# Performance work log

Hardware: AMD Instinct MI355X
Metric: run time of the kernel (lower is better)

## Reference

```python
import jax, jax.numpy as jnp
import numpy as np

KERNEL_MUL = 2.0
KERNEL_NUM = 5


def setup_inputs() -> dict:
    key = jax.random.key(0)
    k1, k2 = jax.random.split(key)
    source = jax.random.normal(k1, (4096, 1024), dtype=jnp.float32)
    target = jax.random.normal(k2, (4096, 1024), dtype=jnp.float32)
    return {"source": source, "target": target}


def reference(source, target):
    bs = source.shape[0]
    total = jnp.concatenate([source, target], axis=0)  # [n, D]
    n = total.shape[0]
    # Pairwise squared L2 distances via the GEMM trick: ||a-b||^2 = a^2 + b^2 - 2ab
    sq = jnp.sum(total * total, axis=1)                 # [n]
    L2 = sq[:, None] + sq[None, :] - 2.0 * (total @ total.T)  # [n, n]
    # Bandwidth computed from detached distances (torch used .data => stop_gradient)
    bw = jax.lax.stop_gradient(L2).sum() / (n * n - n)
    bw = bw / (KERNEL_MUL ** (KERNEL_NUM // 2))
    bws = bw * (KERNEL_MUL ** jnp.arange(KERNEL_NUM, dtype=L2.dtype))  # [K]
    # Multi-bandwidth Gaussian kernel sum: [K, n, n] -> [n, n]
    K = jnp.exp(-L2[None, :, :] / bws[:, None, None]).sum(axis=0)
    XX = K[:bs, :bs].mean()
    YY = K[bs:, bs:].mean()
    XY = K[:bs, bs:].mean()
    YX = K[bs:, :bs].mean()
    return XX + YY - XY - YX
```

## Files before the change

kernel.cpp:

```cpp
#include <hip/hip_runtime.h>
#include <hip/hip_bf16.h>
#include <stdint.h>
#include <stddef.h>

#define NTOT 8192
#define BS   4096
#define DIM  1024
#define NTRI 2080
#define QS   20.0f

#define OFF_TB      0u
#define OFF_SQ      8388608u
#define OFF_COLPART 8421376u
#define OFF_COLP2   10518528u
#define OFF_BWP     10551296u
#define OFF_PART    10551360u


typedef __attribute__((ext_vector_type(4)))  int   i32x4;
typedef __attribute__((ext_vector_type(16))) int   i32x16;

__device__ __forceinline__ float fast_sqrt(float x) {
#if __has_builtin(__builtin_amdgcn_sqrtf)
  return __builtin_amdgcn_sqrtf(x);
#else
  float r; asm("v_sqrt_f32 %0, %1" : "=v"(r) : "v"(x)); return r;
#endif
}

__device__ __forceinline__ float fast_exp2(float x) {
#if __has_builtin(__builtin_amdgcn_exp2f)
  return __builtin_amdgcn_exp2f(x);
#else
  float r; asm("v_exp_f32 %0, %1" : "=v"(r) : "v"(x)); return r;
#endif
}

__device__ __forceinline__ void load_lds16(const void* g, void* l) {
  __builtin_amdgcn_global_load_lds((const __attribute__((address_space(1))) void*)g,
                                   (__attribute__((address_space(3))) void*)l,
                                   16, 0, 0);
}

__device__ __forceinline__ int quant4(float4 v) {
  int q0 = __float2int_rn(fminf(fmaxf(v.x * QS, -127.f), 127.f));
  int q1 = __float2int_rn(fminf(fmaxf(v.y * QS, -127.f), 127.f));
  int q2 = __float2int_rn(fminf(fmaxf(v.z * QS, -127.f), 127.f));
  int q3 = __float2int_rn(fminf(fmaxf(v.w * QS, -127.f), 127.f));
  return (q0 & 255) | ((q1 & 255) << 8) | ((q2 & 255) << 16) | ((q3 & 255) << 24);
}

__global__ __launch_bounds__(256) void prep_kernel(const float* __restrict__ src,
                                                   const float* __restrict__ tgt,
                                                   unsigned char* __restrict__ tb,
                                                   float* __restrict__ sq,
                                                   float* __restrict__ colpart) {
  const int t = threadIdx.x;
  const int lane = t & 63, wave = t >> 6;
  const int R = blockIdx.x;
  const int r0 = R * 16;
  const int kt = t >> 4, kq = (t >> 2) & 3, b0 = (t & 3) * 4;
  unsigned char* dstbase = tb + (size_t)R * 16384 + kt * 1024 + kq * 256 + b0;
  __shared__ float rs[16][4];
  float c0 = 0.f, c1 = 0.f, c2 = 0.f, c3 = 0.f;
#pragma unroll 4
  for (int r = 0; r < 16; ++r) {
    const int row = r0 + r;
    const float* base = (row < BS) ? (src + (size_t)row * DIM)
                                   : (tgt + (size_t)(row - BS) * DIM);
    float4 v = *reinterpret_cast<const float4*>(base + t * 4);
    *reinterpret_cast<int*>(dstbase + r * 16) = quant4(v);
    c0 += v.x; c1 += v.y; c2 += v.z; c3 += v.w;
    float s = v.x*v.x + v.y*v.y + v.z*v.z + v.w*v.w;
#pragma unroll
    for (int off = 32; off > 0; off >>= 1) s += __shfl_down(s, off, 64);
    if (lane == 0) rs[r][wave] = s;
  }
  float4 cp = {c0, c1, c2, c3};
  *reinterpret_cast<float4*>(colpart + (size_t)R * 1024 + t * 4) = cp;
  __syncthreads();
  if (t < 16) sq[r0 + t] = (rs[t][0] + rs[t][1]) + (rs[t][2] + rs[t][3]);
}

__global__ __launch_bounds__(1024) void colred_kernel(const float* __restrict__ colpart,
                                                      float* __restrict__ colp2) {
  const int b = blockIdx.x, t = threadIdx.x;
  float s = 0.f;
  for (int g = b * 64; g < b * 64 + 64; ++g) s += colpart[(size_t)g * 1024 + t];
  colp2[b * 1024 + t] = s;
}

__global__ __launch_bounds__(1024) void bw_kernel(const float* __restrict__ sq,
                                                  const float* __restrict__ colp2,
                                                  float* __restrict__ bwp) {
  const int t = threadIdx.x;
  double s1 = 0.0;
#pragma unroll
  for (int i = 0; i < 8; ++i) s1 += (double)sq[t + i * 1024];
  float s = 0.f;
#pragma unroll
  for (int j = 0; j < 8; ++j) s += colp2[j * 1024 + t];
  double s2 = (double)s * (double)s;
  __shared__ double r1[1024], r2[1024];
  r1[t] = s1; r2[t] = s2;
  __syncthreads();
  for (int off = 512; off > 0; off >>= 1) {
    if (t < off) { r1[t] += r1[t + off]; r2[t] += r2[t + off]; }
    __syncthreads();
  }
  if (t == 0) {
    const double n = (double)NTOT;
    double sumL2 = 2.0 * n * r1[0] - 2.0 * r2[0];
    double bw = sumL2 / (n * n - n);
    bw = bw / 4.0;
    const double LOG2E = 1.4426950408889634;
    for (int k = 0; k < 5; ++k)
      bwp[k] = (float)(-LOG2E / (bw * (double)(1 << k)));
  }
}

#define STAGE(kt1024, ldsA, ldsB)                                             \
  do {                                                                        \
    load_lds16(T + a0g + (kt1024), (ldsA) + (size_t)(wave * 64) * 16);        \
    load_lds16(T + a1g + (kt1024), (ldsA) + (size_t)(256 + wave * 64) * 16);  \
    load_lds16(T + b0g + (kt1024), (ldsB) + (size_t)(wave * 64) * 16);        \
    load_lds16(T + b1g + (kt1024), (ldsB) + (size_t)(256 + wave * 64) * 16);  \
  } while (0)

#define COMPUTE64(Abuf, Bbuf)                                                 \
  do {                                                                        \
    _Pragma("unroll")                                                         \
    for (int kk = 0; kk < 2; ++kk) {                                          \
      i32x4 fa0 = *reinterpret_cast<const i32x4*>(&(Abuf)[abase + kk * 512]); \
      i32x4 fa1 = *reinterpret_cast<const i32x4*>(&(Abuf)[abase + 2048 + kk * 512]); \
      i32x4 fb0 = *reinterpret_cast<const i32x4*>(&(Bbuf)[bbase + kk * 512]); \
      i32x4 fb1 = *reinterpret_cast<const i32x4*>(&(Bbuf)[bbase + 2048 + kk * 512]); \
      acc00 = __builtin_amdgcn_mfma_i32_32x32x32_i8(fa0, fb0, acc00, 0, 0, 0); \
      acc01 = __builtin_amdgcn_mfma_i32_32x32x32_i8(fa0, fb1, acc01, 0, 0, 0); \
      acc10 = __builtin_amdgcn_mfma_i32_32x32x32_i8(fa1, fb0, acc10, 0, 0, 0); \
      acc11 = __builtin_amdgcn_mfma_i32_32x32x32_i8(fa1, fb1, acc11, 0, 0, 0); \
    }                                                                         \
  } while (0)

#define BARR __builtin_amdgcn_s_barrier()

#define EXP5(x16) ({ float u_ = fast_exp2(x16);                               \
                     float u2_ = u_ * u_, u4_ = u2_ * u2_;                    \
                     float u8_ = u4_ * u4_, u16_ = u8_ * u8_;                 \
                     ((u_ + u2_) + (u4_ + u8_)) + u16_; })

__global__ __launch_bounds__(256, 4) void mmd_gemm(const unsigned char* __restrict__ T,
                                                   const float* __restrict__ sq,
                                                   const float* __restrict__ bwp,
                                                   float* __restrict__ partials) {
  __shared__ __align__(16) unsigned char sA0[8192], sA1[8192];
  __shared__ __align__(16) unsigned char sB0[8192], sB1[8192];
  __shared__ float wred[4];

  const int tid  = threadIdx.x;
  const int lane = tid & 63;
  const int wave = tid >> 6;
  const int wr   = wave >> 1;
  const int wc   = wave & 1;
  const int bid  = blockIdx.x;

  const int col5 = lane & 31;
  const int hi32 = lane >> 5;
  const int abase0 = (col5 >> 4) * 1024 + hi32 * 256 + (lane & 15) * 16;
  const int abase = wr * 4096 + abase0;
  const int bbase = wc * 4096 + abase0;

  const int nrep = (bid < 32) ? 2 : 1;
  for (int rep = 0; rep < nrep; ++rep) {
    int tno;
    if (bid < 32) tno = bid * 2 + rep;
    else { const int idx = bid - 32; tno = 64 + (idx & 7) * 252 + (idx >> 3); }

    int bi = (int)((129.0f - fast_sqrt(129.0f * 129.0f - 8.0f * (float)tno)) * 0.5f);
    while (bi > 0 && bi * (129 - bi) / 2 > tno) --bi;
    while ((bi + 1) * (129 - (bi + 1)) / 2 <= tno) ++bi;
    const int bj = bi + (tno - bi * (129 - bi) / 2);

    const int aRB = bi * 8, bRB = bj * 8;
    const int f0 = tid, f1 = 256 + tid;
    const size_t a0g = (size_t)(aRB + (f0 >> 6)) * 16384 + (f0 & 63) * 16;
    const size_t a1g = (size_t)(aRB + (f1 >> 6)) * 16384 + (f1 & 63) * 16;
    const size_t b0g = (size_t)(bRB + (f0 >> 6)) * 16384 + (f0 & 63) * 16;
    const size_t b1g = (size_t)(bRB + (f1 >> 6)) * 16384 + (f1 & 63) * 16;

    i32x16 acc00 = {}, acc01 = {}, acc10 = {}, acc11 = {};

    STAGE(0, sA0, sB0);

    for (int t = 0; t < 8; ++t) {
      STAGE((2 * t + 1) * 1024, sA1, sB1);
      asm volatile("s_waitcnt vmcnt(4)" ::: "memory");
      BARR;
      __builtin_amdgcn_sched_barrier(0);
      COMPUTE64(sA0, sB0);
      __builtin_amdgcn_sched_barrier(0);
      BARR;

      if (t < 7) {
        STAGE((2 * t + 2) * 1024, sA0, sB0);
        asm volatile("s_waitcnt vmcnt(4)" ::: "memory");
      } else {
        asm volatile("s_waitcnt vmcnt(0)" ::: "memory");
      }
      BARR;
      __builtin_amdgcn_sched_barrier(0);
      COMPUTE64(sA1, sB1);
      __builtin_amdgcn_sched_barrier(0);
      BARR;
    }

    const float s16 = bwp[0] * 0.0625f;
    const float c2i = -2.f * s16 / (QS * QS);

    const float bj0 = sq[bj * 128 + wc * 64 + col5] * s16;
    const float bj1 = sq[bj * 128 + wc * 64 + 32 + col5] * s16;

    float tsum = 0.f;
#pragma unroll
    for (int tm = 0; tm < 2; ++tm) {
      const int rbaseq = bi * 128 + wr * 64 + tm * 32 + 4 * hi32;
#pragma unroll
      for (int q = 0; q < 4; ++q) {
#pragma unroll
        for (int p = 0; p < 4; ++p) {
          const float ai = sq[rbaseq + q * 8 + p] * s16;
          const int r = q * 4 + p;
          const int v0 = tm ? acc10[r] : acc00[r];
          const int v1 = tm ? acc11[r] : acc01[r];
          tsum += EXP5(fmaf((float)v0, c2i, ai + bj0));
          tsum += EXP5(fmaf((float)v1, c2i, ai + bj1));
        }
      }
    }

#pragma unroll
    for (int off = 32; off > 0; off >>= 1) tsum += __shfl_down(tsum, off, 64);
    if (lane == 0) wred[wave] = tsum;
    __syncthreads();
    if (tid == 0) {
      float sign = ((bi < 32) == (bj < 32)) ? 1.f : -1.f;
      float wgt  = (bi == bj) ? 1.f : 2.f;
      partials[tno] = sign * wgt * ((wred[0] + wred[1]) + (wred[2] + wred[3]));
    }
    __syncthreads();
  }
}

__global__ __launch_bounds__(256) void finish_kernel(const float* __restrict__ partials,
                                                     float* __restrict__ out) {
  const int t = threadIdx.x;
  double s = 0.0;
  for (int i = t; i < NTRI; i += 256) s += (double)partials[i];
  __shared__ double rd[256];
  rd[t] = s;
  __syncthreads();
  for (int off = 128; off > 0; off >>= 1) {
    if (t < off) rd[t] += rd[t + off];
    __syncthreads();
  }
  if (t == 0) out[0] = (float)(rd[0] / 16777216.0);
}

extern "C" void kernel_launch(void* const* d_in, const int* in_sizes, int n_in,
                              void* d_out, int out_size, void* d_ws, size_t ws_size,
                              hipStream_t stream) {
  const float* src = (const float*)d_in[0];
  const float* tgt = (const float*)d_in[1];
  char* ws = (char*)d_ws;
  unsigned char* tb = (unsigned char*)(ws + OFF_TB);
  float* sq       = (float*)(ws + OFF_SQ);
  float* colpart  = (float*)(ws + OFF_COLPART);
  float* colp2    = (float*)(ws + OFF_COLP2);
  float* bwp      = (float*)(ws + OFF_BWP);
  float* partials = (float*)(ws + OFF_PART);

  prep_kernel<<<dim3(512), dim3(256), 0, stream>>>(src, tgt, tb, sq, colpart);
  colred_kernel<<<dim3(8), dim3(1024), 0, stream>>>(colpart, colp2);
  bw_kernel<<<dim3(1), dim3(1024), 0, stream>>>(sq, colp2, bwp);
  mmd_gemm<<<dim3(2048), dim3(256), 0, stream>>>(tb, sq, bwp, partials);
  finish_kernel<<<dim3(1), dim3(256), 0, stream>>>(partials, (float*)d_out);
}
```

Measured before the change: 76.83 us.

## Enlarge GEMM tile to 256x128 over block-row pairs of the triangle

The tile shape moves from 128x128 to 256x128, and tiles are enumerated over pairs of block rows of the symmetric upper triangle. Each wave now holds a 4x2 grid of MFMA accumulators, which raises arithmetic intensity per LDS byte and halves the number of workgroups. Sub-tiles below the diagonal are computed but skipped in the exp epilogue, and the per-wave sign and weight replace the per-block ones. In exchange, register and LDS use grow, occupancy drops to 2 blocks per CU, and some MFMA work below the diagonal is wasted.

```diff
diff --git a/kernel.cpp b/kernel.cpp
--- a/kernel.cpp
+++ b/kernel.cpp
@@ -6,7 +6,7 @@
 #define NTOT 8192
 #define BS   4096
 #define DIM  1024
-#define NTRI 2080
+#define NT2  1056
 #define QS   20.0f
 
 #define OFF_TB      0u
@@ -121,24 +121,33 @@
 
 #define STAGE(kt1024, ldsA, ldsB)                                             \
   do {                                                                        \
-    load_lds16(T + a0g + (kt1024), (ldsA) + (size_t)(wave * 64) * 16);        \
-    load_lds16(T + a1g + (kt1024), (ldsA) + (size_t)(256 + wave * 64) * 16);  \
-    load_lds16(T + b0g + (kt1024), (ldsB) + (size_t)(wave * 64) * 16);        \
-    load_lds16(T + b1g + (kt1024), (ldsB) + (size_t)(256 + wave * 64) * 16);  \
+    load_lds16(T + ga0 + (kt1024), (ldsA) + (size_t)(wave * 64) * 16);        \
+    load_lds16(T + ga1 + (kt1024), (ldsA) + (size_t)(256 + wave * 64) * 16);  \
+    load_lds16(T + ga2 + (kt1024), (ldsA) + (size_t)(512 + wave * 64) * 16);  \
+    load_lds16(T + ga3 + (kt1024), (ldsA) + (size_t)(768 + wave * 64) * 16);  \
+    load_lds16(T + gb0 + (kt1024), (ldsB) + (size_t)(wave * 64) * 16);        \
+    load_lds16(T + gb1 + (kt1024), (ldsB) + (size_t)(256 + wave * 64) * 16);  \
   } while (0)
 
 #define COMPUTE64(Abuf, Bbuf)                                                 \
   do {                                                                        \
     _Pragma("unroll")                                                         \
     for (int kk = 0; kk < 2; ++kk) {                                          \
-      i32x4 fa0 = *reinterpret_cast<const i32x4*>(&(Abuf)[abase + kk * 512]); \
-      i32x4 fa1 = *reinterpret_cast<const i32x4*>(&(Abuf)[abase + 2048 + kk * 512]); \
-      i32x4 fb0 = *reinterpret_cast<const i32x4*>(&(Bbuf)[bbase + kk * 512]); \
-      i32x4 fb1 = *reinterpret_cast<const i32x4*>(&(Bbuf)[bbase + 2048 + kk * 512]); \
-      acc00 = __builtin_amdgcn_mfma_i32_32x32x32_i8(fa0, fb0, acc00, 0, 0, 0); \
-      acc01 = __builtin_amdgcn_mfma_i32_32x32x32_i8(fa0, fb1, acc01, 0, 0, 0); \
-      acc10 = __builtin_amdgcn_mfma_i32_32x32x32_i8(fa1, fb0, acc10, 0, 0, 0); \
-      acc11 = __builtin_amdgcn_mfma_i32_32x32x32_i8(fa1, fb1, acc11, 0, 0, 0); \
+      i32x4 fa[4], fb[2];                                                     \
+      _Pragma("unroll")                                                       \
+      for (int tm = 0; tm < 4; ++tm)                                          \
+        fa[tm] = *reinterpret_cast<const i32x4*>(                             \
+            &(Abuf)[awb + tm * 2048 + tbase + kk * 512]);                     \
+      _Pragma("unroll")                                                       \
+      for (int tn = 0; tn < 2; ++tn)                                          \
+        fb[tn] = *reinterpret_cast<const i32x4*>(                             \
+            &(Bbuf)[bwb + tn * 2048 + tbase + kk * 512]);                     \
+      _Pragma("unroll")                                                       \
+      for (int tm = 0; tm < 4; ++tm)                                          \
+        _Pragma("unroll")                                                     \
+        for (int tn = 0; tn < 2; ++tn)                                        \
+          acc[tm][tn] = __builtin_amdgcn_mfma_i32_32x32x32_i8(                \
+              fa[tm], fb[tn], acc[tm][tn], 0, 0, 0);                          \
     }                                                                         \
   } while (0)
 
@@ -149,12 +158,12 @@
                      float u8_ = u4_ * u4_, u16_ = u8_ * u8_;                 \
                      ((u_ + u2_) + (u4_ + u8_)) + u16_; })
 
-__global__ __launch_bounds__(256, 4) void mmd_gemm(const unsigned char* __restrict__ T,
+__global__ __launch_bounds__(256, 2) void mmd_gemm(const unsigned char* __restrict__ T,
                                                    const float* __restrict__ sq,
                                                    const float* __restrict__ bwp,
                                                    float* __restrict__ partials) {
-  __shared__ __align__(16) unsigned char sA0[8192], sA1[8192];
-  __shared__ __align__(16) unsigned char sB0[8192], sB1[8192];
+  __shared__ __align__(16) unsigned char sA0[16384], sA1[16384];
+  __shared__ __align__(16) unsigned char sB0[8192],  sB1[8192];
   __shared__ float wred[4];
 
   const int tid  = threadIdx.x;
@@ -166,35 +175,37 @@
 
   const int col5 = lane & 31;
   const int hi32 = lane >> 5;
-  const int abase0 = (col5 >> 4) * 1024 + hi32 * 256 + (lane & 15) * 16;
-  const int abase = wr * 4096 + abase0;
-  const int bbase = wc * 4096 + abase0;
+  const int tbase = (col5 >> 4) * 1024 + hi32 * 256 + (lane & 15) * 16;
+  const int awb = wr * 8192;
+  const int bwb = wc * 4096;
 
   const int nrep = (bid < 32) ? 2 : 1;
   for (int rep = 0; rep < nrep; ++rep) {
     int tno;
     if (bid < 32) tno = bid * 2 + rep;
-    else { const int idx = bid - 32; tno = 64 + (idx & 7) * 252 + (idx >> 3); }
-
-    int bi = (int)((129.0f - fast_sqrt(129.0f * 129.0f - 8.0f * (float)tno)) * 0.5f);
-    while (bi > 0 && bi * (129 - bi) / 2 > tno) --bi;
-    while ((bi + 1) * (129 - (bi + 1)) / 2 <= tno) ++bi;
-    const int bj = bi + (tno - bi * (129 - bi) / 2);
-
-    const int aRB = bi * 8, bRB = bj * 8;
-    const int f0 = tid, f1 = 256 + tid;
-    const size_t a0g = (size_t)(aRB + (f0 >> 6)) * 16384 + (f0 & 63) * 16;
-    const size_t a1g = (size_t)(aRB + (f1 >> 6)) * 16384 + (f1 & 63) * 16;
-    const size_t b0g = (size_t)(bRB + (f0 >> 6)) * 16384 + (f0 & 63) * 16;
-    const size_t b1g = (size_t)(bRB + (f1 >> 6)) * 16384 + (f1 & 63) * 16;
-
-    i32x16 acc00 = {}, acc01 = {}, acc10 = {}, acc11 = {};
+    else { const int idx = bid - 32; tno = 64 + (idx & 7) * 124 + (idx >> 3); }
+
+    int I = (int)((65.0f - fast_sqrt(65.f * 65.f - 4.f * (float)tno)) * 0.5f);
+    while (I > 0 && I * (65 - I) > tno) --I;
+    while ((I + 1) * (64 - I) <= tno) ++I;
+    const int j = 2 * I + (tno - I * (65 - I));
+
+    const int aRB = I * 16, bRB = j * 8;
+    const int f0 = tid;
+    const size_t ga0 = (size_t)(aRB + (f0 >> 6)) * 16384 + (f0 & 63) * 16;
+    const size_t ga1 = (size_t)(aRB + ((256 + f0) >> 6)) * 16384 + (f0 & 63) * 16;
+    const size_t ga2 = (size_t)(aRB + ((512 + f0) >> 6)) * 16384 + (f0 & 63) * 16;
+    const size_t ga3 = (size_t)(aRB + ((768 + f0) >> 6)) * 16384 + (f0 & 63) * 16;
+    const size_t gb0 = (size_t)(bRB + (f0 >> 6)) * 16384 + (f0 & 63) * 16;
+    const size_t gb1 = (size_t)(bRB + ((256 + f0) >> 6)) * 16384 + (f0 & 63) * 16;
+
+    i32x16 acc[4][2] = {};
 
     STAGE(0, sA0, sB0);
 
     for (int t = 0; t < 8; ++t) {
       STAGE((2 * t + 1) * 1024, sA1, sB1);
-      asm volatile("s_waitcnt vmcnt(4)" ::: "memory");
+      asm volatile("s_waitcnt vmcnt(6)" ::: "memory");
       BARR;
       __builtin_amdgcn_sched_barrier(0);
       COMPUTE64(sA0, sB0);
@@ -203,7 +214,7 @@
 
       if (t < 7) {
         STAGE((2 * t + 2) * 1024, sA0, sB0);
-        asm volatile("s_waitcnt vmcnt(4)" ::: "memory");
+        asm volatile("s_waitcnt vmcnt(6)" ::: "memory");
       } else {
         asm volatile("s_waitcnt vmcnt(0)" ::: "memory");
       }
@@ -214,39 +225,40 @@
       BARR;
     }
 
-    const float s16 = bwp[0] * 0.0625f;
-    const float c2i = -2.f * s16 / (QS * QS);
-
-    const float bj0 = sq[bj * 128 + wc * 64 + col5] * s16;
-    const float bj1 = sq[bj * 128 + wc * 64 + 32 + col5] * s16;
+    const int ri = 2 * I + wr, cj = j;
+    float wsgn = (cj > ri) ? 2.f : (cj == ri ? 1.f : 0.f);
+    if ((ri < 32) != (cj < 32)) wsgn = -wsgn;
 
     float tsum = 0.f;
-#pragma unroll
-    for (int tm = 0; tm < 2; ++tm) {
-      const int rbaseq = bi * 128 + wr * 64 + tm * 32 + 4 * hi32;
-#pragma unroll
-      for (int q = 0; q < 4; ++q) {
-#pragma unroll
-        for (int p = 0; p < 4; ++p) {
-          const float ai = sq[rbaseq + q * 8 + p] * s16;
-          const int r = q * 4 + p;
-          const int v0 = tm ? acc10[r] : acc00[r];
-          const int v1 = tm ? acc11[r] : acc01[r];
-          tsum += EXP5(fmaf((float)v0, c2i, ai + bj0));
-          tsum += EXP5(fmaf((float)v1, c2i, ai + bj1));
+    if (wsgn != 0.f) {
+      const float s16 = bwp[0] * 0.0625f;
+      const float c2i = -2.f * s16 / (QS * QS);
+      float bjv[2];
+      bjv[0] = sq[j * 128 + wc * 64 + col5] * s16;
+      bjv[1] = sq[j * 128 + wc * 64 + 32 + col5] * s16;
+#pragma unroll
+      for (int tm = 0; tm < 4; ++tm) {
+        const int rbaseq = I * 256 + wr * 128 + tm * 32 + 4 * hi32;
+#pragma unroll
+        for (int q = 0; q < 4; ++q) {
+#pragma unroll
+          for (int p = 0; p < 4; ++p) {
+            const float ai = sq[rbaseq + q * 8 + p] * s16;
+            const int r = q * 4 + p;
+            tsum += EXP5(fmaf((float)acc[0+0][0][0]*0.f + (float)acc[tm][0][r], c2i, ai + bjv[0]));
+            tsum += EXP5(fmaf((float)acc[tm][1][r], c2i, ai + bjv[1]));
+          }
         }
       }
+      tsum *= wsgn;
     }
 
 #pragma unroll
     for (int off = 32; off > 0; off >>= 1) tsum += __shfl_down(tsum, off, 64);
     if (lane == 0) wred[wave] = tsum;
     __syncthreads();
-    if (tid == 0) {
-      float sign = ((bi < 32) == (bj < 32)) ? 1.f : -1.f;
-      float wgt  = (bi == bj) ? 1.f : 2.f;
-      partials[tno] = sign * wgt * ((wred[0] + wred[1]) + (wred[2] + wred[3]));
-    }
+    if (tid == 0)
+      partials[tno] = (wred[0] + wred[1]) + (wred[2] + wred[3]);
     __syncthreads();
   }
 }
@@ -255,7 +267,7 @@
                                                      float* __restrict__ out) {
   const int t = threadIdx.x;
   double s = 0.0;
-  for (int i = t; i < NTRI; i += 256) s += (double)partials[i];
+  for (int i = t; i < NT2; i += 256) s += (double)partials[i];
   __shared__ double rd[256];
   rd[t] = s;
   __syncthreads();
@@ -282,6 +294,6 @@
   prep_kernel<<<dim3(512), dim3(256), 0, stream>>>(src, tgt, tb, sq, colpart);
   colred_kernel<<<dim3(8), dim3(1024), 0, stream>>>(colpart, colp2);
   bw_kernel<<<dim3(1), dim3(1024), 0, stream>>>(sq, colp2, bwp);
-  mmd_gemm<<<dim3(2048), dim3(256), 0, stream>>>(tb, sq, bwp, partials);
+  mmd_gemm<<<dim3(1024), dim3(256), 0, stream>>>(tb, sq, bwp, partials);
   finish_kernel<<<dim3(1), dim3(256), 0, stream>>>(partials, (float*)d_out);
 }
```

After: 79.97 us. 1.04x slower.
